# Performance work log

Measured on AMD Instinct MI355X. Metric: run time of the kernel, lower is better.

The kernel has to match this reference:

```python
import jax, jax.numpy as jnp
import numpy as np

B, D, NTXT, H = 16384, 512, 4096, 1024


def _linear_params(key, fan_in, fan_out):
    kw, kb = jax.random.split(key)
    s = 1.0 / np.sqrt(fan_in)
    W = jax.random.uniform(kw, (fan_in, fan_out), jnp.float32, -s, s)
    b = jax.random.uniform(kb, (fan_out,), jnp.float32, -s, s)
    return W, b


def setup_inputs() -> dict:
    key = jax.random.key(0)
    ks = jax.random.split(key, 9)
    img_features = jax.random.normal(ks[0], (B, D), jnp.float32)
    txt_features = jax.random.normal(ks[1], (D, NTXT), jnp.float32)
    target_ind = jax.random.randint(ks[2], (B,), 0, NTXT, jnp.int32)
    Wi0, bi0 = _linear_params(ks[3], D, H)
    Wi1, bi1 = _linear_params(ks[4], H, H)
    Wi2, bi2 = _linear_params(ks[5], H, D)
    Wt0, bt0 = _linear_params(ks[6], D, H)
    Wt1, bt1 = _linear_params(ks[7], H, H)
    Wt2, bt2 = _linear_params(ks[8], H, D)
    logit_scale = jnp.asarray(np.log(1.0 / 0.07), jnp.float32)
    temp = jnp.asarray(1.0, jnp.float32)
    return {
        "img_features": img_features, "txt_features": txt_features,
        "target_ind": target_ind, "temp": temp,
        "Wi0": Wi0, "bi0": bi0, "Wi1": Wi1, "bi1": bi1, "Wi2": Wi2, "bi2": bi2,
        "Wt0": Wt0, "bt0": bt0, "Wt1": Wt1, "bt1": bt1, "Wt2": Wt2, "bt2": bt2,
        "logit_scale": logit_scale,
    }


def _mlp(x, params):
    # ReLU after every layer except the last (matches MLP.forward)
    for W, b in params[:-1]:
        x = jax.nn.relu(x @ W + b)
    W, b = params[-1]
    return x @ W + b


def reference(img_features, txt_features, target_ind, temp,
              Wi0, bi0, Wi1, bi1, Wi2, bi2,
              Wt0, bt0, Wt1, bt1, Wt2, bt2, logit_scale):
    p_img = _mlp(img_features, [(Wi0, bi0), (Wi1, bi1), (Wi2, bi2)])          # [B, D]
    p_txt = _mlp(txt_features.T, [(Wt0, bt0), (Wt1, bt1), (Wt2, bt2)])        # [N, D]

    sim = (p_img @ p_txt.T) * jnp.exp(logit_scale)                            # [B, N]
    sim = sim / jnp.linalg.norm(sim, axis=-1, keepdims=True)
    out_logits = sim / jnp.linalg.norm(sim, axis=-1, keepdims=True)           # faithful double-normalize

    # vectorized form of the per-sample Python-loop softmax-CE in MLP_CLIP_loss
    logp = jax.nn.log_softmax(out_logits / temp, axis=-1)                     # [B, N]
    picked = jnp.take_along_axis(logp, target_ind[:, None].astype(jnp.int32), axis=1)[:, 0]
    loss = -jnp.mean(picked)

    # accuracy branch (uses unscaled similarity, row-normalized)
    sim_clip = p_img @ p_txt.T
    sim_clip = sim_clip / jnp.linalg.norm(sim_clip, axis=-1, keepdims=True)
    acc = jnp.sum(jnp.argmax(sim_clip, axis=1).astype(jnp.int32) == target_ind)
    return loss, acc
```

## Files before the change

### kernel.cpp

```cpp
#include <hip/hip_runtime.h>
#include <cstdint>
#include <cstddef>

#define B_ROWS 16384
#define D_DIM  512
#define NTXT_N 4096
#define H_DIM  1024

typedef __attribute__((ext_vector_type(8))) short short8;
typedef __attribute__((ext_vector_type(4))) float f32x4;

__device__ __forceinline__ ushort f2bf(float x) {
    union { float f; uint32_t u; } c; c.f = x;
    const uint32_t u = c.u;
    return (ushort)((u + 0x7fffu + ((u >> 16) & 1u)) >> 16);
}
__device__ __forceinline__ float bf2f(ushort h) {
    union { uint32_t u; float f; } c; c.u = ((uint32_t)h) << 16;
    return c.f;
}

#define GLDS16(gp, lp) __builtin_amdgcn_global_load_lds( \
    (const __attribute__((address_space(1))) void*)(gp),  \
    (__attribute__((address_space(3))) void*)(lp), 16, 0, 0)

__device__ __forceinline__ void xcd_remap(int& bx, int& by) {
    const int nx = gridDim.x, ny = gridDim.y;
    const int nwg = nx * ny;
    const int bid = by * nx + bx;
    const int q = nwg >> 3, r = nwg & 7;
    const int xcd = bid & 7, idx = bid >> 3;
    const int nb = (xcd < r ? xcd * (q + 1) : r * (q + 1) + (xcd - r) * q) + idx;
    bx = nb % nx; by = nb / nx;
}

__global__ void init_kernel(int* acc) {
    if (threadIdx.x == 0 && blockIdx.x == 0) *acc = 0;
}

__global__ void tsplit_kernel(const float* __restrict__ in, ushort* __restrict__ oh,
                              ushort* __restrict__ ol, int R, int C, int cbase)
{
    __shared__ float tile[32][33];
    const int c0 = blockIdx.x * 32, r0 = blockIdx.y * 32;
    const int tx = threadIdx.x, ty = threadIdx.y;
    #pragma unroll
    for (int j = 0; j < 32; j += 8)
        tile[ty + j][tx] = in[(size_t)(r0 + ty + j) * C + cbase + c0 + tx];
    __syncthreads();
    #pragma unroll
    for (int j = 0; j < 32; j += 8) {
        const float v = tile[tx][ty + j];
        const ushort h = f2bf(v);
        const size_t idx = (size_t)(c0 + ty + j) * R + r0 + tx;
        oh[idx] = h;
        ol[idx] = f2bf(v - bf2f(h));
    }
}

__global__ void csplit_kernel(const float* __restrict__ in, ushort* __restrict__ oh,
                              ushort* __restrict__ ol, int n)
{
    const int i = (blockIdx.x * 256 + threadIdx.x) * 4;
    if (i >= n) return;
    const float4 f = *(const float4*)&in[i];
    ushort4 h, l;
    h.x = f2bf(f.x); l.x = f2bf(f.x - bf2f(h.x));
    h.y = f2bf(f.y); l.y = f2bf(f.y - bf2f(h.y));
    h.z = f2bf(f.z); l.z = f2bf(f.z - bf2f(h.z));
    h.w = f2bf(f.w); l.w = f2bf(f.w - bf2f(h.w));
    *(ushort4*)&oh[i] = h;
    *(ushort4*)&ol[i] = l;
}

template<int K, int OMODE, bool RELU, bool BIAS>
__global__ __launch_bounds__(256, 2)
void gemm_p2_kernel(const ushort* __restrict__ Ah, const ushort* __restrict__ Al,
                    const ushort* __restrict__ Bh, const ushort* __restrict__ Bl,
                    const float* __restrict__ bias,
                    float* __restrict__ Cf, ushort* __restrict__ Ch, ushort* __restrict__ Cl,
                    int M, int N)
{
    constexpr int NT = K / 32;
    __shared__ __align__(16) ushort LDSB[2 * 4 * 4096];

    const int tid  = threadIdx.x;
    const int lane = tid & 63;
    const int w    = tid >> 6;
    const int wr   = w >> 1, wc = w & 1;

    int bxi = blockIdx.x, byi = blockIdx.y;
    xcd_remap(bxi, byi);
    const int bm = byi * 128, bn = bxi * 128;

    const int    stlo  = w * 1024;
    const int    srow  = w * 32 + (lane >> 2);
    const int    scol  = (((lane & 3) ^ ((lane >> 3) & 3)) << 3);
    const size_t aoff0 = (size_t)(bm + srow) * K + scol;
    const size_t boff0 = (size_t)(bn + srow) * K + scol;

    const int frow = lane & 15;
    const int koff = ((lane >> 4) ^ ((frow >> 1) & 3)) << 3;

    f32x4 acc[4][4];
    #pragma unroll
    for (int m = 0; m < 4; ++m)
        #pragma unroll
        for (int n = 0; n < 4; ++n)
            acc[m][n] = (f32x4)0.0f;

#define STAGE(tt, bi) do {                                                    \
        const int _kk = (tt) * 32;                                            \
        ushort* _b = &LDSB[(bi) * 16384];                                     \
        GLDS16(Ah + aoff0 + _kk,          _b +         stlo);                 \
        GLDS16(Ah + aoff0 + _kk + 16 * K, _b +         stlo + 512);           \
        GLDS16(Al + aoff0 + _kk,          _b +  4096 + stlo);                 \
        GLDS16(Al + aoff0 + _kk + 16 * K, _b +  4096 + stlo + 512);           \
        GLDS16(Bh + boff0 + _kk,          _b +  8192 + stlo);                 \
        GLDS16(Bh + boff0 + _kk + 16 * K, _b +  8192 + stlo + 512);           \
        GLDS16(Bl + boff0 + _kk,          _b + 12288 + stlo);                 \
        GLDS16(Bl + boff0 + _kk + 16 * K, _b + 12288 + stlo + 512);           \
    } while (0)

#define COMPUTE(bi) do {                                                      \
        const ushort* _Ahs = &LDSB[(bi) * 16384];                             \
        const ushort* _Als = _Ahs + 4096;                                     \
        const ushort* _Bhs = _Ahs + 8192;                                     \
        const ushort* _Bls = _Ahs + 12288;                                    \
        short8 a_h[4], a_l[4], b_h[4], b_l[4];                                \
        _Pragma("unroll")                                                     \
        for (int m = 0; m < 4; ++m) {                                         \
            const int off = (wr * 64 + m * 16 + frow) * 32 + koff;            \
            a_h[m] = *(const short8*)&_Ahs[off];                              \
            a_l[m] = *(const short8*)&_Als[off];                              \
        }                                                                     \
        _Pragma("unroll")                                                     \
        for (int n = 0; n < 4; ++n) {                                         \
            const int off = (wc * 64 + n * 16 + frow) * 32 + koff;            \
            b_h[n] = *(const short8*)&_Bhs[off];                              \
            b_l[n] = *(const short8*)&_Bls[off];                              \
        }                                                                     \
        __builtin_amdgcn_s_setprio(1);                                        \
        _Pragma("unroll")                                                     \
        for (int m = 0; m < 4; ++m)                                           \
            _Pragma("unroll")                                                 \
            for (int n = 0; n < 4; ++n) {                                     \
                acc[m][n] = __builtin_amdgcn_mfma_f32_16x16x32_bf16(          \
                    a_h[m], b_h[n], acc[m][n], 0, 0, 0);                      \
                acc[m][n] = __builtin_amdgcn_mfma_f32_16x16x32_bf16(          \
                    a_h[m], b_l[n], acc[m][n], 0, 0, 0);                      \
                acc[m][n] = __builtin_amdgcn_mfma_f32_16x16x32_bf16(          \
                    a_l[m], b_h[n], acc[m][n], 0, 0, 0);                      \
            }                                                                 \
        __builtin_amdgcn_s_setprio(0);                                        \
    } while (0)

    STAGE(0, 0);
    #pragma unroll 2
    for (int t = 0; t < NT; ++t) {
        __syncthreads();
        if (t + 1 < NT) STAGE(t + 1, (t + 1) & 1);
        COMPUTE(t & 1);
    }

#undef STAGE
#undef COMPUTE

    const int crow0 = bm + wr * 64 + (lane >> 4) * 4;
    const int ccol0 = bn + wc * 64 + (lane & 15);
    #pragma unroll
    for (int m = 0; m < 4; ++m)
        #pragma unroll
        for (int n = 0; n < 4; ++n) {
            const int col = ccol0 + n * 16;
            const float bv = BIAS ? bias[col] : 0.0f;
            #pragma unroll
            for (int q = 0; q < 4; ++q) {
                float v = acc[m][n][q] + bv;
                if (RELU) v = fmaxf(v, 0.0f);
                const size_t idx = (size_t)(crow0 + m * 16 + q) * N + col;
                if (OMODE == 0) {
                    Cf[idx] = v;
                } else {
                    const ushort h = f2bf(v);
                    Ch[idx] = h;
                    Cl[idx] = f2bf(v - bf2f(h));
                }
            }
        }
}

__global__ __launch_bounds__(256) void rowreduce_kernel(
    const float* __restrict__ sim, const int* __restrict__ tgt,
    const float* __restrict__ temp_p, float* __restrict__ perrow,
    int* __restrict__ acc_cnt, int row0)
{
    const int row = blockIdx.x;
    const float* srow = sim + (size_t)row * NTXT_N;
    const int tid = threadIdx.x;

    float v[16];
    #pragma unroll
    for (int q = 0; q < 4; ++q) {
        float4 f = *(const float4*)&srow[4 * tid + 1024 * q];
        v[4 * q + 0] = f.x; v[4 * q + 1] = f.y; v[4 * q + 2] = f.z; v[4 * q + 3] = f.w;
    }

    float ss = 0.0f, mx = -3.4e38f; int mi = 0x7fffffff;
    #pragma unroll
    for (int q = 0; q < 4; ++q)
        #pragma unroll
        for (int r = 0; r < 4; ++r) {
            const int j = 4 * tid + 1024 * q + r;
            const float x = v[4 * q + r];
            ss = fmaf(x, x, ss);
            if (x > mx) { mx = x; mi = j; }
            else if (x == mx && j < mi) mi = j;
        }

    #pragma unroll
    for (int off = 32; off; off >>= 1) {
        ss += __shfl_down(ss, off);
        const float omx = __shfl_down(mx, off);
        const int   omi = __shfl_down(mi, off);
        if (omx > mx || (omx == mx && omi < mi)) { mx = omx; mi = omi; }
    }

    __shared__ float sws[4], swm[4];
    __shared__ int   swi[4];
    __shared__ float bC, bMx;
    __shared__ int   bAmax;
    const int w = tid >> 6, lane = tid & 63;
    if (lane == 0) { sws[w] = ss; swm[w] = mx; swi[w] = mi; }
    __syncthreads();
    if (tid == 0) {
        float tss = 0.0f, tmx = -3.4e38f; int tmi = 0x7fffffff;
        #pragma unroll
        for (int i = 0; i < 4; ++i) {
            tss += sws[i];
            if (swm[i] > tmx || (swm[i] == tmx && swi[i] < tmi)) { tmx = swm[i]; tmi = swi[i]; }
        }
        const float inv_nr = 1.0f / sqrtf(tss);
        const float n2 = sqrtf(tss * inv_nr * inv_nr);
        const float Cv = inv_nr / (n2 * temp_p[0]);
        bC = Cv; bMx = tmx * Cv; bAmax = tmi;
    }
    __syncthreads();
    const float Cv = bC, mxx = bMx;

    float es = 0.0f;
    #pragma unroll
    for (int q = 0; q < 16; ++q) es += expf(v[q] * Cv - mxx);
    #pragma unroll
    for (int off = 32; off; off >>= 1) es += __shfl_down(es, off);
    if (lane == 0) sws[w] = es;
    __syncthreads();
    if (tid == 0) {
        const float tes = sws[0] + sws[1] + sws[2] + sws[3];
        const float lse = mxx + logf(tes);
        const int t = tgt[row0 + row];
        perrow[row0 + row] = lse - srow[t] * Cv;
        if (bAmax == t) atomicAdd(acc_cnt, 1);
    }
}

__global__ __launch_bounds__(256) void finalize_kernel(
    const float* __restrict__ perrow, const int* __restrict__ acc_cnt,
    float* __restrict__ out)
{
    __shared__ float red[256];
    const int tid = threadIdx.x;
    float s = 0.0f;
    for (int i = tid; i < B_ROWS; i += 256) s += perrow[i];
    red[tid] = s;
    __syncthreads();
    for (int st = 128; st; st >>= 1) {
        if (tid < st) red[tid] += red[tid + st];
        __syncthreads();
    }
    if (tid == 0) {
        out[0] = red[0] / (float)B_ROWS;
        out[1] = (float)(*acc_cnt);
    }
}

extern "C" void kernel_launch(void* const* d_in, const int* in_sizes, int n_in,
                              void* d_out, int out_size, void* d_ws, size_t ws_size,
                              hipStream_t stream)
{
    const float* img  = (const float*)d_in[0];
    const float* txt  = (const float*)d_in[1];
    const int*   tgt  = (const int*)  d_in[2];
    const float* temp = (const float*)d_in[3];
    const float* Wf[6] = { (const float*)d_in[4],  (const float*)d_in[6],  (const float*)d_in[8],
                           (const float*)d_in[10], (const float*)d_in[12], (const float*)d_in[14] };
    const float* bf[6] = { (const float*)d_in[5],  (const float*)d_in[7],  (const float*)d_in[9],
                           (const float*)d_in[11], (const float*)d_in[13], (const float*)d_in[15] };
    float* out = (float*)d_out;

    const int wK[6] = { D_DIM, H_DIM, H_DIM, D_DIM, H_DIM, H_DIM };
    const int wN[6] = { H_DIM, H_DIM, D_DIM, H_DIM, H_DIM, D_DIM };

    auto need = [&](size_t ch, size_t sc) -> size_t {
        size_t wt = 0;
        for (int i = 0; i < 6; ++i) wt += (size_t)wK[i] * wN[i] * 2 * 2;
        const size_t a01 = 2 * (ch * H_DIM * 2 * 2);
        const size_t pt  = (size_t)NTXT_N * D_DIM * 2 * 2;
        const size_t sim = sc * NTXT_N * 4;
        return wt + a01 + pt + sim + (size_t)B_ROWS * 4 + (size_t)64 * 1024;
    };
    const size_t ladder[][2] = { {16384, 4096}, {16384, 2048}, {8192, 4096}, {8192, 2048},
                                 {4096, 2048},  {4096, 1024},  {2048, 1024}, {1024, 1024} };
    size_t CH = 1024, SIMCH = 512;
    for (auto& e : ladder)
        if (need(e[0], e[1]) <= ws_size) { CH = e[0]; SIMCH = e[1]; break; }

    uint8_t* p = (uint8_t*)d_ws;
    auto alloc = [&](size_t bytes) -> void* {
        void* r = (void*)p; p += (bytes + 255) & ~(size_t)255; return r;
    };
    ushort* WTh[6]; ushort* WTl[6];
    for (int i = 0; i < 6; ++i) {
        WTh[i] = (ushort*)alloc((size_t)wK[i] * wN[i] * 2);
        WTl[i] = (ushort*)alloc((size_t)wK[i] * wN[i] * 2);
    }
    ushort* A0h = (ushort*)alloc(CH * H_DIM * 2);
    ushort* A0l = (ushort*)alloc(CH * H_DIM * 2);
    ushort* A1h = (ushort*)alloc(CH * H_DIM * 2);
    ushort* A1l = (ushort*)alloc(CH * H_DIM * 2);
    ushort* PTh = (ushort*)alloc((size_t)NTXT_N * D_DIM * 2);
    ushort* PTl = (ushort*)alloc((size_t)NTXT_N * D_DIM * 2);
    float*  SIM = (float*)alloc(SIMCH * NTXT_N * 4);
    float*  PERROW = (float*)alloc((size_t)B_ROWS * 4);
    int*    ACC = (int*)alloc(64);
    ushort* XBh = A1h;  ushort* XBl = A1l;
    ushort* PIh = A0h;  ushort* PIl = A0l;

    init_kernel<<<1, 64, 0, stream>>>(ACC);

    for (int i = 0; i < 6; ++i)
        tsplit_kernel<<<dim3(wN[i] / 32, wK[i] / 32), dim3(32, 8), 0, stream>>>(
            Wf[i], WTh[i], WTl[i], wK[i], wN[i], 0);

    const size_t CHT = CH < (size_t)NTXT_N ? CH : (size_t)NTXT_N;
    for (size_t n0 = 0; n0 < NTXT_N; n0 += CHT) {
        tsplit_kernel<<<dim3(CHT / 32, D_DIM / 32), dim3(32, 8), 0, stream>>>(
            txt, XBh, XBl, D_DIM, NTXT_N, (int)n0);
        gemm_p2_kernel<D_DIM, 1, true, true><<<dim3(H_DIM / 128, CHT / 128), 256, 0, stream>>>(
            XBh, XBl, WTh[3], WTl[3], bf[3], nullptr, A0h, A0l, (int)CHT, H_DIM);
        gemm_p2_kernel<H_DIM, 1, true, true><<<dim3(H_DIM / 128, CHT / 128), 256, 0, stream>>>(
            A0h, A0l, WTh[4], WTl[4], bf[4], nullptr, A1h, A1l, (int)CHT, H_DIM);
        gemm_p2_kernel<H_DIM, 1, false, true><<<dim3(D_DIM / 128, CHT / 128), 256, 0, stream>>>(
            A1h, A1l, WTh[5], WTl[5], bf[5], nullptr,
            PTh + n0 * D_DIM, PTl + n0 * D_DIM, (int)CHT, D_DIM);
    }

    for (size_t m0 = 0; m0 < B_ROWS; m0 += CH) {
        csplit_kernel<<<(CH * D_DIM / 4 + 255) / 256, 256, 0, stream>>>(
            img + m0 * D_DIM, XBh, XBl, (int)(CH * D_DIM));
        gemm_p2_kernel<D_DIM, 1, true, true><<<dim3(H_DIM / 128, CH / 128), 256, 0, stream>>>(
            XBh, XBl, WTh[0], WTl[0], bf[0], nullptr, A0h, A0l, (int)CH, H_DIM);
        gemm_p2_kernel<H_DIM, 1, true, true><<<dim3(H_DIM / 128, CH / 128), 256, 0, stream>>>(
            A0h, A0l, WTh[1], WTl[1], bf[1], nullptr, A1h, A1l, (int)CH, H_DIM);
        gemm_p2_kernel<H_DIM, 1, false, true><<<dim3(D_DIM / 128, CH / 128), 256, 0, stream>>>(
            A1h, A1l, WTh[2], WTl[2], bf[2], nullptr, PIh, PIl, (int)CH, D_DIM);
        for (size_t s0 = 0; s0 < CH; s0 += SIMCH) {
            gemm_p2_kernel<D_DIM, 0, false, false><<<dim3(NTXT_N / 128, SIMCH / 128), 256, 0, stream>>>(
                PIh + s0 * D_DIM, PIl + s0 * D_DIM, PTh, PTl, nullptr,
                SIM, nullptr, nullptr, (int)SIMCH, NTXT_N);
            rowreduce_kernel<<<SIMCH, 256, 0, stream>>>(
                SIM, tgt, temp, PERROW, ACC, (int)(m0 + s0));
        }
    }

    finalize_kernel<<<1, 256, 0, stream>>>(PERROW, ACC, out);
}
```

Measured before the change: 706.0 us.

## Pre-pack B operands into MFMA fragment layout and load them directly from global

Weights and the text projection output are repacked into a fragment-ordered layout so each lane reads its B-operand short8 straight from global/L2 instead of staging B through LDS. This halves the LDS footprint per block, which allows occupancy to rise to 3 blocks per CU. The cost is that B loads are no longer shared across the block via LDS, so each wave refetches B from cache. The third text-MLP GEMM also gets a scattered packed-layout epilogue.

```diff
diff --git a/kernel.cpp b/kernel.cpp
--- a/kernel.cpp
+++ b/kernel.cpp
@@ -73,16 +73,39 @@
     *(ushort4*)&ol[i] = l;
 }
 
+__global__ void wpack_kernel(const float* __restrict__ in, ushort* __restrict__ oh,
+                             ushort* __restrict__ ol, int K, int N)
+{
+    __shared__ float tile[32][33];
+    const int n0 = blockIdx.x * 32, k0 = blockIdx.y * 32;
+    const int tid = threadIdx.x;
+    const int r = tid >> 3, c4 = (tid & 7) << 2;
+    const float4 f = *(const float4*)&in[(size_t)(k0 + r) * N + n0 + c4];
+    tile[r][c4 + 0] = f.x; tile[r][c4 + 1] = f.y; tile[r][c4 + 2] = f.z; tile[r][c4 + 3] = f.w;
+    __syncthreads();
+    const int hl = tid & 1, lane = (tid >> 1) & 63, nbl = tid >> 7;
+    const int frow = lane & 15, ks = lane >> 4;
+    short8 v;
+    #pragma unroll
+    for (int j = 0; j < 8; ++j) {
+        const float x = tile[ks * 8 + j][nbl * 16 + frow];
+        const ushort h = f2bf(x);
+        v[j] = (short)(hl ? f2bf(x - bf2f(h)) : h);
+    }
+    const size_t dst = (((size_t)(n0 / 16 + nbl) * (K >> 5) + (k0 >> 5)) * 64 + lane) * 8;
+    *(short8*)&((hl ? ol : oh)[dst]) = v;
+}
+
 template<int K, int OMODE, bool RELU, bool BIAS>
-__global__ __launch_bounds__(256, 2)
-void gemm_p2_kernel(const ushort* __restrict__ Ah, const ushort* __restrict__ Al,
-                    const ushort* __restrict__ Bh, const ushort* __restrict__ Bl,
+__global__ __launch_bounds__(256, 3)
+void gemm_bd_kernel(const ushort* __restrict__ Ah, const ushort* __restrict__ Al,
+                    const ushort* __restrict__ PBh, const ushort* __restrict__ PBl,
                     const float* __restrict__ bias,
                     float* __restrict__ Cf, ushort* __restrict__ Ch, ushort* __restrict__ Cl,
-                    int M, int N)
+                    int rowoff, int M, int N)
 {
     constexpr int NT = K / 32;
-    __shared__ __align__(16) ushort LDSB[2 * 4 * 4096];
+    __shared__ __align__(16) ushort LDSB[2 * 8192];
 
     const int tid  = threadIdx.x;
     const int lane = tid & 63;
@@ -92,12 +115,12 @@
     int bxi = blockIdx.x, byi = blockIdx.y;
     xcd_remap(bxi, byi);
     const int bm = byi * 128, bn = bxi * 128;
+    const int bnb = bn >> 4;
 
     const int    stlo  = w * 1024;
     const int    srow  = w * 32 + (lane >> 2);
     const int    scol  = (((lane & 3) ^ ((lane >> 3) & 3)) << 3);
     const size_t aoff0 = (size_t)(bm + srow) * K + scol;
-    const size_t boff0 = (size_t)(bn + srow) * K + scol;
 
     const int frow = lane & 15;
     const int koff = ((lane >> 4) ^ ((frow >> 1) & 3)) << 3;
@@ -111,34 +134,29 @@
 
 #define STAGE(tt, bi) do {                                                    \
         const int _kk = (tt) * 32;                                            \
-        ushort* _b = &LDSB[(bi) * 16384];                                     \
-        GLDS16(Ah + aoff0 + _kk,          _b +         stlo);                 \
-        GLDS16(Ah + aoff0 + _kk + 16 * K, _b +         stlo + 512);           \
-        GLDS16(Al + aoff0 + _kk,          _b +  4096 + stlo);                 \
-        GLDS16(Al + aoff0 + _kk + 16 * K, _b +  4096 + stlo + 512);           \
-        GLDS16(Bh + boff0 + _kk,          _b +  8192 + stlo);                 \
-        GLDS16(Bh + boff0 + _kk + 16 * K, _b +  8192 + stlo + 512);           \
-        GLDS16(Bl + boff0 + _kk,          _b + 12288 + stlo);                 \
-        GLDS16(Bl + boff0 + _kk + 16 * K, _b + 12288 + stlo + 512);           \
+        ushort* _b = &LDSB[(bi) * 8192];                                      \
+        GLDS16(Ah + aoff0 + _kk,          _b +        stlo);                  \
+        GLDS16(Ah + aoff0 + _kk + 16 * K, _b +        stlo + 512);            \
+        GLDS16(Al + aoff0 + _kk,          _b + 4096 + stlo);                  \
+        GLDS16(Al + aoff0 + _kk + 16 * K, _b + 4096 + stlo + 512);            \
     } while (0)
 
-#define COMPUTE(bi) do {                                                      \
-        const ushort* _Ahs = &LDSB[(bi) * 16384];                             \
+#define COMPUTE(tt, bi) do {                                                  \
+        const ushort* _Ahs = &LDSB[(bi) * 8192];                              \
         const ushort* _Als = _Ahs + 4096;                                     \
-        const ushort* _Bhs = _Ahs + 8192;                                     \
-        const ushort* _Bls = _Ahs + 12288;                                    \
         short8 a_h[4], a_l[4], b_h[4], b_l[4];                                \
+        _Pragma("unroll")                                                     \
+        for (int n = 0; n < 4; ++n) {                                         \
+            const size_t bidx =                                               \
+                (((size_t)(bnb + wc * 4 + n) * NT + (tt)) * 64 + lane) * 8;   \
+            b_h[n] = *(const short8*)&PBh[bidx];                              \
+            b_l[n] = *(const short8*)&PBl[bidx];                              \
+        }                                                                     \
         _Pragma("unroll")                                                     \
         for (int m = 0; m < 4; ++m) {                                         \
             const int off = (wr * 64 + m * 16 + frow) * 32 + koff;            \
             a_h[m] = *(const short8*)&_Ahs[off];                              \
             a_l[m] = *(const short8*)&_Als[off];                              \
-        }                                                                     \
-        _Pragma("unroll")                                                     \
-        for (int n = 0; n < 4; ++n) {                                         \
-            const int off = (wc * 64 + n * 16 + frow) * 32 + koff;            \
-            b_h[n] = *(const short8*)&_Bhs[off];                              \
-            b_l[n] = *(const short8*)&_Bls[off];                              \
         }                                                                     \
         __builtin_amdgcn_s_setprio(1);                                        \
         _Pragma("unroll")                                                     \
@@ -160,7 +178,7 @@
     for (int t = 0; t < NT; ++t) {
         __syncthreads();
         if (t + 1 < NT) STAGE(t + 1, (t + 1) & 1);
-        COMPUTE(t & 1);
+        COMPUTE(t, t & 1);
     }
 
 #undef STAGE
@@ -168,6 +186,7 @@
 
     const int crow0 = bm + wr * 64 + (lane >> 4) * 4;
     const int ccol0 = bn + wc * 64 + (lane & 15);
+    const int NTo = N >> 5;
     #pragma unroll
     for (int m = 0; m < 4; ++m)
         #pragma unroll
@@ -178,13 +197,22 @@
             for (int q = 0; q < 4; ++q) {
                 float v = acc[m][n][q] + bv;
                 if (RELU) v = fmaxf(v, 0.0f);
-                const size_t idx = (size_t)(crow0 + m * 16 + q) * N + col;
                 if (OMODE == 0) {
-                    Cf[idx] = v;
-                } else {
+                    Cf[(size_t)(crow0 + m * 16 + q) * N + col] = v;
+                } else if (OMODE == 1) {
+                    const size_t idx = (size_t)(crow0 + m * 16 + q) * N + col;
                     const ushort h = f2bf(v);
                     Ch[idx] = h;
                     Cl[idx] = f2bf(v - bf2f(h));
+                } else {
+                    const int gr = rowoff + crow0 + m * 16 + q;
+                    const int nb2 = gr >> 4, fr2 = gr & 15;
+                    const int tt2 = col >> 5, ks2 = (col >> 3) & 3, jj = col & 7;
+                    const size_t pidx =
+                        (((size_t)nb2 * NTo + tt2) * 64 + fr2 + (ks2 << 4)) * 8 + jj;
+                    const ushort h = f2bf(v);
+                    Ch[pidx] = h;
+                    Cl[pidx] = f2bf(v - bf2f(h));
                 }
             }
         }
@@ -319,10 +347,10 @@
     auto alloc = [&](size_t bytes) -> void* {
         void* r = (void*)p; p += (bytes + 255) & ~(size_t)255; return r;
     };
-    ushort* WTh[6]; ushort* WTl[6];
+    ushort* PWh[6]; ushort* PWl[6];
     for (int i = 0; i < 6; ++i) {
-        WTh[i] = (ushort*)alloc((size_t)wK[i] * wN[i] * 2);
-        WTl[i] = (ushort*)alloc((size_t)wK[i] * wN[i] * 2);
+        PWh[i] = (ushort*)alloc((size_t)wK[i] * wN[i] * 2);
+        PWl[i] = (ushort*)alloc((size_t)wK[i] * wN[i] * 2);
     }
     ushort* A0h = (ushort*)alloc(CH * H_DIM * 2);
     ushort* A0l = (ushort*)alloc(CH * H_DIM * 2);
@@ -339,35 +367,34 @@
     init_kernel<<<1, 64, 0, stream>>>(ACC);
 
     for (int i = 0; i < 6; ++i)
-        tsplit_kernel<<<dim3(wN[i] / 32, wK[i] / 32), dim3(32, 8), 0, stream>>>(
-            Wf[i], WTh[i], WTl[i], wK[i], wN[i], 0);
+        wpack_kernel<<<dim3(wN[i] / 32, wK[i] / 32), 256, 0, stream>>>(
+            Wf[i], PWh[i], PWl[i], wK[i], wN[i]);
 
     const size_t CHT = CH < (size_t)NTXT_N ? CH : (size_t)NTXT_N;
     for (size_t n0 = 0; n0 < NTXT_N; n0 += CHT) {
         tsplit_kernel<<<dim3(CHT / 32, D_DIM / 32), dim3(32, 8), 0, stream>>>(
             txt, XBh, XBl, D_DIM, NTXT_N, (int)n0);
-        gemm_p2_kernel<D_DIM, 1, true, true><<<dim3(H_DIM / 128, CHT / 128), 256, 0, stream>>>(
-            XBh, XBl, WTh[3], WTl[3], bf[3], nullptr, A0h, A0l, (int)CHT, H_DIM);
-        gemm_p2_kernel<H_DIM, 1, true, true><<<dim3(H_DIM / 128, CHT / 128), 256, 0, stream>>>(
-            A0h, A0l, WTh[4], WTl[4], bf[4], nullptr, A1h, A1l, (int)CHT, H_DIM);
-        gemm_p2_kernel<H_DIM, 1, false, true><<<dim3(D_DIM / 128, CHT / 128), 256, 0, stream>>>(
-            A1h, A1l, WTh[5], WTl[5], bf[5], nullptr,
-            PTh + n0 * D_DIM, PTl + n0 * D_DIM, (int)CHT, D_DIM);
+        gemm_bd_kernel<D_DIM, 1, true, true><<<dim3(H_DIM / 128, CHT / 128), 256, 0, stream>>>(
+            XBh, XBl, PWh[3], PWl[3], bf[3], nullptr, A0h, A0l, 0, (int)CHT, H_DIM);
+        gemm_bd_kernel<H_DIM, 1, true, true><<<dim3(H_DIM / 128, CHT / 128), 256, 0, stream>>>(
+            A0h, A0l, PWh[4], PWl[4], bf[4], nullptr, A1h, A1l, 0, (int)CHT, H_DIM);
+        gemm_bd_kernel<H_DIM, 2, false, true><<<dim3(D_DIM / 128, CHT / 128), 256, 0, stream>>>(
+            A1h, A1l, PWh[5], PWl[5], bf[5], nullptr, PTh, PTl, (int)n0, (int)CHT, D_DIM);
     }
 
     for (size_t m0 = 0; m0 < B_ROWS; m0 += CH) {
         csplit_kernel<<<(CH * D_DIM / 4 + 255) / 256, 256, 0, stream>>>(
             img + m0 * D_DIM, XBh, XBl, (int)(CH * D_DIM));
-        gemm_p2_kernel<D_DIM, 1, true, true><<<dim3(H_DIM / 128, CH / 128), 256, 0, stream>>>(
-            XBh, XBl, WTh[0], WTl[0], bf[0], nullptr, A0h, A0l, (int)CH, H_DIM);
-        gemm_p2_kernel<H_DIM, 1, true, true><<<dim3(H_DIM / 128, CH / 128), 256, 0, stream>>>(
-            A0h, A0l, WTh[1], WTl[1], bf[1], nullptr, A1h, A1l, (int)CH, H_DIM);
-        gemm_p2_kernel<H_DIM, 1, false, true><<<dim3(D_DIM / 128, CH / 128), 256, 0, stream>>>(
-            A1h, A1l, WTh[2], WTl[2], bf[2], nullptr, PIh, PIl, (int)CH, D_DIM);
+        gemm_bd_kernel<D_DIM, 1, true, true><<<dim3(H_DIM / 128, CH / 128), 256, 0, stream>>>(
+            XBh, XBl, PWh[0], PWl[0], bf[0], nullptr, A0h, A0l, 0, (int)CH, H_DIM);
+        gemm_bd_kernel<H_DIM, 1, true, true><<<dim3(H_DIM / 128, CH / 128), 256, 0, stream>>>(
+            A0h, A0l, PWh[1], PWl[1], bf[1], nullptr, A1h, A1l, 0, (int)CH, H_DIM);
+        gemm_bd_kernel<H_DIM, 1, false, true><<<dim3(D_DIM / 128, CH / 128), 256, 0, stream>>>(
+            A1h, A1l, PWh[2], PWl[2], bf[2], nullptr, PIh, PIl, 0, (int)CH, D_DIM);
         for (size_t s0 = 0; s0 < CH; s0 += SIMCH) {
-            gemm_p2_kernel<D_DIM, 0, false, false><<<dim3(NTXT_N / 128, SIMCH / 128), 256, 0, stream>>>(
+            gemm_bd_kernel<D_DIM, 0, false, false><<<dim3(NTXT_N / 128, SIMCH / 128), 256, 0, stream>>>(
                 PIh + s0 * D_DIM, PIl + s0 * D_DIM, PTh, PTl, nullptr,
-                SIM, nullptr, nullptr, (int)SIMCH, NTXT_N);
+                SIM, nullptr, nullptr, 0, (int)SIMCH, NTXT_N);
             rowreduce_kernel<<<SIMCH, 256, 0, stream>>>(
                 SIM, tgt, temp, PERROW, ACC, (int)(m0 + s0));
         }
```

Result: slower. 732.4 us (+3.7%).

## Add 256x256-tile split-bf16 GEMM kernel for large image-MLP and similarity GEMMs

Applied to the files above, without the earlier changes.

Adds a 512-thread GEMM kernel with 256x256 output tiles and double-buffered LDS staging. Each wave computes a 128x64 sub-tile using the 3-term hi/lo bf16 MFMA product. It is used for the first two image-MLP layers and the similarity GEMM when the chunk sizes are large enough, with the 128-tile kernel kept as a fallback. Larger tiles are meant to raise operand reuse per byte loaded from global memory. The cost is heavy register pressure (128 accumulator floats per lane), 128KB of LDS per block, and fewer blocks in the grid.

```diff
diff --git a/kernel.cpp b/kernel.cpp
--- a/kernel.cpp
+++ b/kernel.cpp
@@ -190,6 +190,123 @@
         }
 }
 
+template<int K, int OMODE, bool RELU, bool BIAS>
+__global__ __launch_bounds__(512, 2)
+void gemm256_kernel(const ushort* __restrict__ Ah, const ushort* __restrict__ Al,
+                    const ushort* __restrict__ Bh, const ushort* __restrict__ Bl,
+                    const float* __restrict__ bias,
+                    float* __restrict__ Cf, ushort* __restrict__ Ch, ushort* __restrict__ Cl,
+                    int M, int N)
+{
+    constexpr int NT = K / 32;
+    __shared__ __align__(16) ushort LDSB[2 * 4 * 8192];
+
+    const int tid  = threadIdx.x;
+    const int lane = tid & 63;
+    const int w    = tid >> 6;
+    const int wr   = w >> 2, wc = w & 3;
+
+    int bxi = blockIdx.x, byi = blockIdx.y;
+    xcd_remap(bxi, byi);
+    const int bm = byi * 256, bn = bxi * 256;
+
+    const int    srow  = tid >> 2;
+    const int    scol  = (((tid & 3) ^ ((tid >> 3) & 3)) << 3);
+    const size_t aoffA = (size_t)(bm + srow) * K + scol;
+    const size_t aoffB = (size_t)(bm + 128 + srow) * K + scol;
+    const size_t boffA = (size_t)(bn + srow) * K + scol;
+    const size_t boffB = (size_t)(bn + 128 + srow) * K + scol;
+    const int    dst   = srow * 32 + (tid & 3) * 8;
+
+    const int frow = lane & 15;
+    const int koff = ((lane >> 4) ^ ((frow >> 1) & 3)) << 3;
+
+    f32x4 acc[8][4];
+    #pragma unroll
+    for (int m = 0; m < 8; ++m)
+        #pragma unroll
+        for (int n = 0; n < 4; ++n)
+            acc[m][n] = (f32x4)0.0f;
+
+#define STAGE256(tt, bi) do {                                                 \
+        const int _kk = (tt) * 32;                                            \
+        ushort* _b = &LDSB[(bi) * 32768];                                     \
+        GLDS16(Ah + aoffA + _kk, _b +         dst);                           \
+        GLDS16(Ah + aoffB + _kk, _b +         dst + 4096);                    \
+        GLDS16(Al + aoffA + _kk, _b +  8192 + dst);                           \
+        GLDS16(Al + aoffB + _kk, _b +  8192 + dst + 4096);                    \
+        GLDS16(Bh + boffA + _kk, _b + 16384 + dst);                           \
+        GLDS16(Bh + boffB + _kk, _b + 16384 + dst + 4096);                    \
+        GLDS16(Bl + boffA + _kk, _b + 24576 + dst);                           \
+        GLDS16(Bl + boffB + _kk, _b + 24576 + dst + 4096);                    \
+    } while (0)
+
+#define COMPUTE256(bi) do {                                                   \
+        const ushort* _Ahs = &LDSB[(bi) * 32768];                             \
+        const ushort* _Als = _Ahs + 8192;                                     \
+        const ushort* _Bhs = _Ahs + 16384;                                    \
+        const ushort* _Bls = _Ahs + 24576;                                    \
+        short8 b_h[4], b_l[4];                                                \
+        _Pragma("unroll")                                                     \
+        for (int n = 0; n < 4; ++n) {                                         \
+            const int off = (wc * 64 + n * 16 + frow) * 32 + koff;            \
+            b_h[n] = *(const short8*)&_Bhs[off];                              \
+            b_l[n] = *(const short8*)&_Bls[off];                              \
+        }                                                                     \
+        __builtin_amdgcn_s_setprio(1);                                        \
+        _Pragma("unroll")                                                     \
+        for (int m = 0; m < 8; ++m) {                                         \
+            const int off = (wr * 128 + m * 16 + frow) * 32 + koff;           \
+            const short8 a_h = *(const short8*)&_Ahs[off];                    \
+            const short8 a_l = *(const short8*)&_Als[off];                    \
+            _Pragma("unroll")                                                 \
+            for (int n = 0; n < 4; ++n) {                                     \
+                acc[m][n] = __builtin_amdgcn_mfma_f32_16x16x32_bf16(          \
+                    a_h, b_h[n], acc[m][n], 0, 0, 0);                         \
+                acc[m][n] = __builtin_amdgcn_mfma_f32_16x16x32_bf16(          \
+                    a_h, b_l[n], acc[m][n], 0, 0, 0);                         \
+                acc[m][n] = __builtin_amdgcn_mfma_f32_16x16x32_bf16(          \
+                    a_l, b_h[n], acc[m][n], 0, 0, 0);                         \
+            }                                                                 \
+        }                                                                     \
+        __builtin_amdgcn_s_setprio(0);                                        \
+    } while (0)
+
+    STAGE256(0, 0);
+    #pragma unroll 2
+    for (int t = 0; t < NT; ++t) {
+        __syncthreads();
+        if (t + 1 < NT) STAGE256(t + 1, (t + 1) & 1);
+        COMPUTE256(t & 1);
+    }
+
+#undef STAGE256
+#undef COMPUTE256
+
+    const int crow0 = bm + wr * 128 + (lane >> 4) * 4;
+    const int ccol0 = bn + wc * 64 + (lane & 15);
+    #pragma unroll
+    for (int m = 0; m < 8; ++m)
+        #pragma unroll
+        for (int n = 0; n < 4; ++n) {
+            const int col = ccol0 + n * 16;
+            const float bv = BIAS ? bias[col] : 0.0f;
+            #pragma unroll
+            for (int q = 0; q < 4; ++q) {
+                float v = acc[m][n][q] + bv;
+                if (RELU) v = fmaxf(v, 0.0f);
+                const size_t idx = (size_t)(crow0 + m * 16 + q) * N + col;
+                if (OMODE == 0) {
+                    Cf[idx] = v;
+                } else {
+                    const ushort h = f2bf(v);
+                    Ch[idx] = h;
+                    Cl[idx] = f2bf(v - bf2f(h));
+                }
+            }
+        }
+}
+
 __global__ __launch_bounds__(256) void rowreduce_kernel(
     const float* __restrict__ sim, const int* __restrict__ tgt,
     const float* __restrict__ temp_p, float* __restrict__ perrow,
@@ -355,19 +472,33 @@
             PTh + n0 * D_DIM, PTl + n0 * D_DIM, (int)CHT, D_DIM);
     }
 
+    const bool big = (CH % 256 == 0) && (CH >= 4096);
     for (size_t m0 = 0; m0 < B_ROWS; m0 += CH) {
         csplit_kernel<<<(CH * D_DIM / 4 + 255) / 256, 256, 0, stream>>>(
             img + m0 * D_DIM, XBh, XBl, (int)(CH * D_DIM));
-        gemm_p2_kernel<D_DIM, 1, true, true><<<dim3(H_DIM / 128, CH / 128), 256, 0, stream>>>(
-            XBh, XBl, WTh[0], WTl[0], bf[0], nullptr, A0h, A0l, (int)CH, H_DIM);
-        gemm_p2_kernel<H_DIM, 1, true, true><<<dim3(H_DIM / 128, CH / 128), 256, 0, stream>>>(
-            A0h, A0l, WTh[1], WTl[1], bf[1], nullptr, A1h, A1l, (int)CH, H_DIM);
+        if (big) {
+            gemm256_kernel<D_DIM, 1, true, true><<<dim3(H_DIM / 256, CH / 256), 512, 0, stream>>>(
+                XBh, XBl, WTh[0], WTl[0], bf[0], nullptr, A0h, A0l, (int)CH, H_DIM);
+            gemm256_kernel<H_DIM, 1, true, true><<<dim3(H_DIM / 256, CH / 256), 512, 0, stream>>>(
+                A0h, A0l, WTh[1], WTl[1], bf[1], nullptr, A1h, A1l, (int)CH, H_DIM);
+        } else {
+            gemm_p2_kernel<D_DIM, 1, true, true><<<dim3(H_DIM / 128, CH / 128), 256, 0, stream>>>(
+                XBh, XBl, WTh[0], WTl[0], bf[0], nullptr, A0h, A0l, (int)CH, H_DIM);
+            gemm_p2_kernel<H_DIM, 1, true, true><<<dim3(H_DIM / 128, CH / 128), 256, 0, stream>>>(
+                A0h, A0l, WTh[1], WTl[1], bf[1], nullptr, A1h, A1l, (int)CH, H_DIM);
+        }
         gemm_p2_kernel<H_DIM, 1, false, true><<<dim3(D_DIM / 128, CH / 128), 256, 0, stream>>>(
             A1h, A1l, WTh[2], WTl[2], bf[2], nullptr, PIh, PIl, (int)CH, D_DIM);
         for (size_t s0 = 0; s0 < CH; s0 += SIMCH) {
-            gemm_p2_kernel<D_DIM, 0, false, false><<<dim3(NTXT_N / 128, SIMCH / 128), 256, 0, stream>>>(
-                PIh + s0 * D_DIM, PIl + s0 * D_DIM, PTh, PTl, nullptr,
-                SIM, nullptr, nullptr, (int)SIMCH, NTXT_N);
+            if ((SIMCH % 256 == 0) && SIMCH >= 2048) {
+                gemm256_kernel<D_DIM, 0, false, false><<<dim3(NTXT_N / 256, SIMCH / 256), 512, 0, stream>>>(
+                    PIh + s0 * D_DIM, PIl + s0 * D_DIM, PTh, PTl, nullptr,
+                    SIM, nullptr, nullptr, (int)SIMCH, NTXT_N);
+            } else {
+                gemm_p2_kernel<D_DIM, 0, false, false><<<dim3(NTXT_N / 128, SIMCH / 128), 256, 0, stream>>>(
+                    PIh + s0 * D_DIM, PIl + s0 * D_DIM, PTh, PTl, nullptr,
+                    SIM, nullptr, nullptr, (int)SIMCH, NTXT_N);
+            }
             rowreduce_kernel<<<SIMCH, 256, 0, stream>>>(
                 SIM, tgt, temp, PERROW, ACC, (int)(m0 + s0));
         }
```

New measurement: 659.7 us. -6.6%, faster.
